# Optimization experiments

Measured on AMD Instinct MI355X. Metric: run time of the kernel, lower is better.

The kernel has to match this reference:

```python
import jax, jax.numpy as jnp
import numpy as np
import math

SCALES = [1, 2, 4, 8]
H = 1024           # hidden_size
NS = len(SCALES)
DS = H // NS       # per-scale dim = 256
NH_S = max(1, 8 // NS)  # heads per scale = 2


def _avg_pool(x, s):
    # x: [B, L, d], kernel=stride=s (L divisible by s)
    B, L, d = x.shape
    return x.reshape(B, L // s, s, d).mean(axis=2)


def _mha(q, k, v, in_w, in_b, out_w, out_b, nh):
    # torch nn.MultiheadAttention, batch_first, no mask.
    d = q.shape[-1]
    wq, wk, wv = in_w[:d], in_w[d:2 * d], in_w[2 * d:]
    bq, bk, bv = in_b[:d], in_b[d:2 * d], in_b[2 * d:]
    qh = q @ wq.T + bq
    kh = k @ wk.T + bk
    vh = v @ wv.T + bv
    B, Lq, _ = qh.shape
    Lk = kh.shape[1]
    hd = d // nh
    qh = qh.reshape(B, Lq, nh, hd).transpose(0, 2, 1, 3)
    kh = kh.reshape(B, Lk, nh, hd).transpose(0, 2, 1, 3)
    vh = vh.reshape(B, Lk, nh, hd).transpose(0, 2, 1, 3)
    scores = jnp.einsum('bhqd,bhkd->bhqk', qh, kh) * (1.0 / math.sqrt(hd))
    w = jax.nn.softmax(scores, axis=-1)
    out = jnp.einsum('bhqk,bhkd->bhqd', w, vh)
    out = out.transpose(0, 2, 1, 3).reshape(B, Lq, d)
    out = out @ out_w.T + out_b
    return out, w.mean(axis=1)  # averaged attn weights (torch default)


def setup_inputs() -> dict:
    key = jax.random.key(0)
    ks = jax.random.split(key, 20)
    B, S = 4, 2048
    f = lambda k, shape: (jax.random.normal(k, shape, dtype=jnp.float32) * 0.02)
    return {
        'query': jax.random.normal(ks[0], (B, S, H), dtype=jnp.float32),
        'key': jax.random.normal(ks[1], (B, S, H), dtype=jnp.float32),
        'value': jax.random.normal(ks[2], (B, S, H), dtype=jnp.float32),
        'wq': f(ks[3], (H, H)), 'bq': f(ks[4], (H,)),
        'wk': f(ks[5], (H, H)), 'bk': f(ks[6], (H,)),
        'wv': f(ks[7], (H, H)), 'bv': f(ks[8], (H,)),
        'mha_in_w': f(ks[9], (NS, 3 * DS, DS)),
        'mha_in_b': f(ks[10], (NS, 3 * DS)),
        'mha_out_w': f(ks[11], (NS, DS, DS)),
        'mha_out_b': f(ks[12], (NS, DS)),
        'fus_w': f(ks[13], (H, H)), 'fus_b': f(ks[14], (H,)),
    }


def reference(query, key, value, wq, bq, wk, bk, wv, bv,
              mha_in_w, mha_in_b, mha_out_w, mha_out_b, fus_w, fus_b):
    q = query @ wq.T + bq
    k = key @ wk.T + bk
    v = value @ wv.T + bv
    outs = []
    weights0 = None
    for i, s in enumerate(SCALES):
        qs = q[..., i * DS:(i + 1) * DS]
        ks_ = k[..., i * DS:(i + 1) * DS]
        vs = v[..., i * DS:(i + 1) * DS]
        if s > 1:
            ks_ = _avg_pool(ks_, s)
            vs = _avg_pool(vs, s)
        attended, w = _mha(qs, ks_, vs, mha_in_w[i], mha_in_b[i],
                           mha_out_w[i], mha_out_b[i], NH_S)
        # F.interpolate back to seq_len is an identity here (query length == seq_len)
        outs.append(attended)
        if i == 0:
            weights0 = w
    fused = jnp.concatenate(outs, axis=-1) @ fus_w.T + fus_b
    return fused, weights0
```

## Files before the change

kernel.cpp:

```cpp
#include <hip/hip_runtime.h>
#include <stdint.h>

typedef unsigned short u16;
typedef __bf16 v8bf __attribute__((ext_vector_type(8)));
typedef float v4f __attribute__((ext_vector_type(4)));
typedef __attribute__((address_space(3))) unsigned lds_t;
typedef const __attribute__((address_space(1))) unsigned g_t;

__device__ __forceinline__ u16 f2bf(float f) {
  union { float f; unsigned u; } v; v.f = f;
  unsigned r = v.u + 0x7FFFu + ((v.u >> 16) & 1u);
  return (u16)(r >> 16);
}
__device__ __forceinline__ float bf2f(u16 h) {
  union { unsigned u; float f; } v; v.u = ((unsigned)h) << 16;
  return v.f;
}
__device__ __forceinline__ ushort4 f4bf(float4 f) {
  ushort4 o;
  o.x = f2bf(f.x); o.y = f2bf(f.y); o.z = f2bf(f.z); o.w = f2bf(f.w);
  return o;
}

__global__ void k_cvt(const float* __restrict__ s, u16* __restrict__ d, long n) {
  long i = ((long)blockIdx.x * blockDim.x + threadIdx.x) * 4;
  long stride = (long)gridDim.x * blockDim.x * 4;
  for (; i < n; i += stride) {
    *(ushort4*)(d + i) = f4bf(*(const float4*)(s + i));
  }
}

__global__ void k_cvtpool(const float* __restrict__ src, u16* __restrict__ dst) {
  int g = blockIdx.x & 255, b = blockIdx.x >> 8;
  int c = threadIdx.x * 4;
  const float* p = src + ((long)b * 2048 + g * 8) * 1024 + c;
  u16* df = dst + ((long)b * 2048 + g * 8) * 1024 + c;
  float4 x[8];
#pragma unroll
  for (int j = 0; j < 8; j++) {
    x[j] = *(const float4*)(p + (long)j * 1024);
    *(ushort4*)(df + (long)j * 1024) = f4bf(x[j]);
  }
  float4 s2[4], s4[2], s8;
#pragma unroll
  for (int j = 0; j < 4; j++) {
    s2[j].x = x[2 * j].x + x[2 * j + 1].x;
    s2[j].y = x[2 * j].y + x[2 * j + 1].y;
    s2[j].z = x[2 * j].z + x[2 * j + 1].z;
    s2[j].w = x[2 * j].w + x[2 * j + 1].w;
  }
#pragma unroll
  for (int j = 0; j < 2; j++) {
    s4[j].x = s2[2 * j].x + s2[2 * j + 1].x;
    s4[j].y = s2[2 * j].y + s2[2 * j + 1].y;
    s4[j].z = s2[2 * j].z + s2[2 * j + 1].z;
    s4[j].w = s2[2 * j].w + s2[2 * j + 1].w;
  }
  s8.x = s4[0].x + s4[1].x; s8.y = s4[0].y + s4[1].y;
  s8.z = s4[0].z + s4[1].z; s8.w = s4[0].w + s4[1].w;
  u16* d2 = dst + ((long)8192 + b * 1024 + g * 4) * 1024 + c;
#pragma unroll
  for (int j = 0; j < 4; j++) {
    float4 t = {s2[j].x * 0.5f, s2[j].y * 0.5f, s2[j].z * 0.5f, s2[j].w * 0.5f};
    *(ushort4*)(d2 + (long)j * 1024) = f4bf(t);
  }
  u16* d4 = dst + ((long)12288 + b * 512 + g * 2) * 1024 + c;
#pragma unroll
  for (int j = 0; j < 2; j++) {
    float4 t = {s4[j].x * 0.25f, s4[j].y * 0.25f, s4[j].z * 0.25f, s4[j].w * 0.25f};
    *(ushort4*)(d4 + (long)j * 1024) = f4bf(t);
  }
  float4 t8 = {s8.x * 0.125f, s8.y * 0.125f, s8.z * 0.125f, s8.w * 0.125f};
  *(ushort4*)(dst + ((long)14336 + b * 256 + g) * 1024 + c) = f4bf(t8);
}

__global__ void k_tc(const float* __restrict__ src, u16* __restrict__ dst, int R, int C) {
  __shared__ float t[32][33];
  long zoff = (long)blockIdx.z * R * C;
  int r0 = blockIdx.y * 32, c0 = blockIdx.x * 32;
  int tx = threadIdx.x & 31, ty = threadIdx.x >> 5;
#pragma unroll
  for (int j = 0; j < 32; j += 8)
    t[ty + j][tx] = src[zoff + (long)(r0 + ty + j) * C + c0 + tx];
  __syncthreads();
#pragma unroll
  for (int j = 0; j < 32; j += 8)
    dst[zoff + (long)(c0 + ty + j) * R + r0 + tx] = f2bf(t[tx][ty + j]);
}

__global__ void k_bcomb_qkv(const float* __restrict__ in_w, const float* __restrict__ in_b,
                            const float* __restrict__ bq, const float* __restrict__ bk,
                            const float* __restrict__ bv, float* __restrict__ out) {
  int gw = (blockIdx.x * 256 + threadIdx.x) >> 6;
  int lane = threadIdx.x & 63;
  int p = gw >> 10, j = gw & 1023, i = j >> 8, of = j & 255;
  const float* bp = p == 0 ? bq : p == 1 ? bk : bv;
  const float* row = in_w + ((long)i * 768 + p * 256 + of) * 256;
  float s = 0.f;
#pragma unroll
  for (int m = 0; m < 4; m++) s += row[lane + m * 64] * bp[i * 256 + lane + m * 64];
#pragma unroll
  for (int m = 32; m >= 1; m >>= 1) s += __shfl_xor(s, m, 64);
  if (lane == 0) out[gw] = in_b[(long)i * 768 + p * 256 + of] + s;
}

__global__ void k_bcomb_f(const float* __restrict__ fw, const float* __restrict__ fb,
                          const float* __restrict__ ob, float* __restrict__ out) {
  int w = (blockIdx.x * 256 + threadIdx.x) >> 6;
  int lane = threadIdx.x & 63;
  const float* row = fw + (long)w * 1024;
  float s = 0.f;
  for (int k = lane; k < 1024; k += 64) s += row[k] * ob[k];
#pragma unroll
  for (int m = 32; m >= 1; m >>= 1) s += __shfl_xor(s, m, 64);
  if (lane == 0) out[w] = fb[w] + s;
}

template<int KS>
__global__ __launch_bounds__(256) void k_ksum(const float* __restrict__ P,
                                              u16* __restrict__ O, long n, int coloff) {
  long i = ((long)blockIdx.x * 256 + threadIdx.x) * 4;
  if (i >= n) return;
  float4 s = *(const float4*)(P + i);
#pragma unroll
  for (int ks = 1; ks < KS; ks++) {
    float4 t = *(const float4*)(P + (long)ks * n + i);
    s.x += t.x; s.y += t.y; s.z += t.z; s.w += t.w;
  }
  *(ushort4*)(O + (i >> 8) * 1024 + coloff + (int)(i & 255)) = f4bf(s);
}

__global__ __launch_bounds__(256) void k_ml0(
    const u16* __restrict__ QHf, const u16* __restrict__ KH,
    float* __restrict__ Mp, float* __restrict__ Lp)
{
  int kc = blockIdx.x;
  int z = blockIdx.z;
  int b = z >> 1, h = z & 1;
  int q0 = blockIdx.y * 64;
  __shared__ u16 KV[2][128][32];
  __shared__ float red[2][4][64];

  const int tid = threadIdx.x, lane = tid & 63, wave = tid >> 6;
  const int q4 = lane >> 4, l16 = lane & 15;
  const int wr = (wave >> 1) * 32, wc = (wave & 1) * 64;
  const int srow = wave * 16 + (lane >> 2), scol = (lane & 3) * 8;
  const float alpha = 0.08838834764831845f;

  v8bf qf[2][4];
#pragma unroll
  for (int mi = 0; mi < 2; mi++)
#pragma unroll
    for (int sub = 0; sub < 4; sub++)
      qf[mi][sub] = *(const v8bf*)(QHf + ((long)b * 2048 + q0 + wr + mi * 16 + l16) * 1024
                                   + h * 128 + sub * 32 + q4 * 8);

  const u16* gK = KH + (long)b * 2048 * 256 + h * 128;
  auto stageK = [&](int buf, int kt, int sub) {
    const u16* g = gK + (long)(kt * 128 + srow) * 256 + sub * 32 + scol;
    __builtin_amdgcn_global_load_lds((g_t*)g, (lds_t*)&KV[buf][wave * 16][0], 16, 0, 0);
    __builtin_amdgcn_global_load_lds((g_t*)(g + 64 * 256), (lds_t*)&KV[buf][64 + wave * 16][0], 16, 0, 0);
  };

  float m_run[2][4], l_run[2][4];
#pragma unroll
  for (int mi = 0; mi < 2; mi++)
#pragma unroll
    for (int i4 = 0; i4 < 4; i4++) { m_run[mi][i4] = -1e30f; l_run[mi][i4] = 0.f; }

  for (int kt = kc * 2; kt < kc * 2 + 2; kt++) {
    v4f s[2][4];
#pragma unroll
    for (int mi = 0; mi < 2; mi++)
#pragma unroll
      for (int ni = 0; ni < 4; ni++) s[mi][ni] = (v4f){0.f, 0.f, 0.f, 0.f};
    stageK(0, kt, 0);
    __syncthreads();
    int cur = 0;
#pragma unroll
    for (int sub = 0; sub < 4; sub++) {
      if (sub < 3) stageK(cur ^ 1, kt, sub + 1);
      v8bf kf[4];
#pragma unroll
      for (int ni = 0; ni < 4; ni++)
        kf[ni] = *(const v8bf*)&KV[cur][wc + ni * 16 + l16][q4 * 8];
#pragma unroll
      for (int mi = 0; mi < 2; mi++)
#pragma unroll
        for (int ni = 0; ni < 4; ni++)
          s[mi][ni] = __builtin_amdgcn_mfma_f32_16x16x32_bf16(qf[mi][sub], kf[ni], s[mi][ni], 0, 0, 0);
      __syncthreads();
      cur ^= 1;
    }
#pragma unroll
    for (int mi = 0; mi < 2; mi++)
#pragma unroll
      for (int ni = 0; ni < 4; ni++) s[mi][ni] *= alpha;
    float mloc[2][4];
#pragma unroll
    for (int mi = 0; mi < 2; mi++)
#pragma unroll
      for (int i4 = 0; i4 < 4; i4++)
        mloc[mi][i4] = fmaxf(fmaxf(s[mi][0][i4], s[mi][1][i4]),
                             fmaxf(s[mi][2][i4], s[mi][3][i4]));
#pragma unroll
    for (int d = 1; d <= 8; d <<= 1)
#pragma unroll
      for (int mi = 0; mi < 2; mi++)
#pragma unroll
        for (int i4 = 0; i4 < 4; i4++)
          mloc[mi][i4] = fmaxf(mloc[mi][i4], __shfl_xor(mloc[mi][i4], d, 64));
    if (l16 == 0) {
#pragma unroll
      for (int mi = 0; mi < 2; mi++)
#pragma unroll
        for (int i4 = 0; i4 < 4; i4++)
          red[0][wave][wr + mi * 16 + q4 * 4 + i4] = mloc[mi][i4];
    }
    __syncthreads();
    float lloc[2][4] = {{0.f, 0.f, 0.f, 0.f}, {0.f, 0.f, 0.f, 0.f}};
#pragma unroll
    for (int mi = 0; mi < 2; mi++)
#pragma unroll
      for (int i4 = 0; i4 < 4; i4++) {
        int rr = wr + mi * 16 + q4 * 4 + i4;
        float mn = fmaxf(fmaxf(red[0][wave][rr], red[0][wave ^ 1][rr]), m_run[mi][i4]);
        float scl = __expf(m_run[mi][i4] - mn);
        m_run[mi][i4] = mn;
        l_run[mi][i4] *= scl;
#pragma unroll
        for (int ni = 0; ni < 4; ni++)
          lloc[mi][i4] += __expf(s[mi][ni][i4] - mn);
      }
#pragma unroll
    for (int d = 1; d <= 8; d <<= 1)
#pragma unroll
      for (int mi = 0; mi < 2; mi++)
#pragma unroll
        for (int i4 = 0; i4 < 4; i4++)
          lloc[mi][i4] += __shfl_xor(lloc[mi][i4], d, 64);
    if (l16 == 0) {
#pragma unroll
      for (int mi = 0; mi < 2; mi++)
#pragma unroll
        for (int i4 = 0; i4 < 4; i4++)
          red[1][wave][wr + mi * 16 + q4 * 4 + i4] = lloc[mi][i4];
    }
    __syncthreads();
#pragma unroll
    for (int mi = 0; mi < 2; mi++)
#pragma unroll
      for (int i4 = 0; i4 < 4; i4++) {
        int rr = wr + mi * 16 + q4 * 4 + i4;
        l_run[mi][i4] += red[1][wave][rr] + red[1][wave ^ 1][rr];
      }
    __syncthreads();
  }

  if ((wave & 1) == 0 && l16 == 0) {
    long zo = ((long)kc * 8 + z) * 2048;
#pragma unroll
    for (int mi = 0; mi < 2; mi++)
#pragma unroll
      for (int i4 = 0; i4 < 4; i4++) {
        int r = q0 + wr + mi * 16 + q4 * 4 + i4;
        Mp[zo + r] = m_run[mi][i4];
        Lp[zo + r] = l_run[mi][i4];
      }
  }
}

__global__ __launch_bounds__(256) void k_mlcomb(
    const float* __restrict__ Mp, const float* __restrict__ Lp,
    float* __restrict__ M0, float* __restrict__ L0)
{
  long r = (long)blockIdx.x * 256 + threadIdx.x;
  float m = -1e30f;
#pragma unroll
  for (int kc = 0; kc < 8; kc++) m = fmaxf(m, Mp[kc * 16384 + r]);
  float l = 0.f;
#pragma unroll
  for (int kc = 0; kc < 8; kc++)
    l += Lp[kc * 16384 + r] * __expf(Mp[kc * 16384 + r] - m);
  M0[r] = m; L0[r] = l;
}

__global__ __launch_bounds__(256) void k_pv0(
    const u16* __restrict__ QHf, const u16* __restrict__ KH,
    const u16* __restrict__ VHT, const float* __restrict__ M0,
    const float* __restrict__ L0, float* __restrict__ PP, float* __restrict__ W0)
{
  int kc = blockIdx.x;
  int b = blockIdx.z;
  int q0 = blockIdx.y * 32;
  __shared__ u16 P[2][32][136];
  __shared__ u16 KV[2][2][128][32];

  const int tid = threadIdx.x, lane = tid & 63, wave = tid >> 6;
  const int q4 = lane >> 4, l16 = lane & 15;
  const int wr = (wave >> 1) * 16, wc = (wave & 1) * 64;
  const int srow = wave * 16 + (lane >> 2), scol = (lane & 3) * 8;
  const float alpha = 0.08838834764831845f;

  float mv[2][4], il[2][4];
#pragma unroll
  for (int h = 0; h < 2; h++)
#pragma unroll
    for (int i4 = 0; i4 < 4; i4++) {
      long r = (long)(b * 2 + h) * 2048 + q0 + wr + q4 * 4 + i4;
      mv[h][i4] = M0[r];
      il[h][i4] = 1.0f / L0[r];
    }

  const u16* gK = KH + (long)b * 2048 * 256;
  const u16* gQ = QHf + ((long)b * 2048 + q0 + wr + l16) * 1024;

  auto stageK2 = [&](int buf, int kt, int sub) {
#pragma unroll
    for (int h = 0; h < 2; h++) {
      const u16* g = gK + (long)(kt * 128 + srow) * 256 + h * 128 + sub * 32 + scol;
      __builtin_amdgcn_global_load_lds((g_t*)g, (lds_t*)&KV[buf][h][wave * 16][0], 16, 0, 0);
      __builtin_amdgcn_global_load_lds((g_t*)(g + 64 * 256), (lds_t*)&KV[buf][h][64 + wave * 16][0], 16, 0, 0);
    }
  };
  auto stageV2 = [&](int buf, int kt, int sub) {
#pragma unroll
    for (int h = 0; h < 2; h++) {
      const u16* g = VHT + ((long)(b * 2 + h) * 128 + srow) * 2048 + kt * 128 + sub * 32 + scol;
      __builtin_amdgcn_global_load_lds((g_t*)g, (lds_t*)&KV[buf][h][wave * 16][0], 16, 0, 0);
      __builtin_amdgcn_global_load_lds((g_t*)(g + (long)64 * 2048), (lds_t*)&KV[buf][h][64 + wave * 16][0], 16, 0, 0);
    }
  };

  v4f acc[2][4];
#pragma unroll
  for (int h = 0; h < 2; h++)
#pragma unroll
    for (int ni = 0; ni < 4; ni++) acc[h][ni] = (v4f){0.f, 0.f, 0.f, 0.f};

  for (int kt = kc * 2; kt < kc * 2 + 2; kt++) {
    v4f s[2][4];
#pragma unroll
    for (int h = 0; h < 2; h++)
#pragma unroll
      for (int ni = 0; ni < 4; ni++) s[h][ni] = (v4f){0.f, 0.f, 0.f, 0.f};
    stageK2(0, kt, 0);
    __syncthreads();
    int cur = 0;
#pragma unroll
    for (int sub = 0; sub < 4; sub++) {
      if (sub < 3) stageK2(cur ^ 1, kt, sub + 1);
      v8bf q2[2], kf[2][4];
#pragma unroll
      for (int h = 0; h < 2; h++)
        q2[h] = *(const v8bf*)(gQ + h * 128 + sub * 32 + q4 * 8);
#pragma unroll
      for (int h = 0; h < 2; h++)
#pragma unroll
        for (int ni = 0; ni < 4; ni++)
          kf[h][ni] = *(const v8bf*)&KV[cur][h][wc + ni * 16 + l16][q4 * 8];
#pragma unroll
      for (int h = 0; h < 2; h++)
#pragma unroll
        for (int ni = 0; ni < 4; ni++)
          s[h][ni] = __builtin_amdgcn_mfma_f32_16x16x32_bf16(q2[h], kf[h][ni], s[h][ni], 0, 0, 0);
      __syncthreads();
      cur ^= 1;
    }
#pragma unroll
    for (int ni = 0; ni < 4; ni++)
#pragma unroll
      for (int i4 = 0; i4 < 4; i4++) {
        float p0 = __expf(s[0][ni][i4] * alpha - mv[0][i4]) * il[0][i4];
        float p1 = __expf(s[1][ni][i4] * alpha - mv[1][i4]) * il[1][i4];
        int rr = wr + q4 * 4 + i4, cc = wc + ni * 16 + l16;
        P[0][rr][cc] = f2bf(p0);
        P[1][rr][cc] = f2bf(p1);
        W0[((long)b * 2048 + q0 + rr) * 2048 + kt * 128 + cc] = 0.5f * (p0 + p1);
      }
    stageV2(0, kt, 0);
    __syncthreads();
    int cv = 0;
#pragma unroll
    for (int sub = 0; sub < 4; sub++) {
      if (sub < 3) stageV2(cv ^ 1, kt, sub + 1);
      v8bf pf[2], vf[2][4];
#pragma unroll
      for (int h = 0; h < 2; h++)
        pf[h] = *(const v8bf*)&P[h][wr + l16][sub * 32 + q4 * 8];
#pragma unroll
      for (int h = 0; h < 2; h++)
#pragma unroll
        for (int ni = 0; ni < 4; ni++)
          vf[h][ni] = *(const v8bf*)&KV[cv][h][wc + ni * 16 + l16][q4 * 8];
#pragma unroll
      for (int h = 0; h < 2; h++)
#pragma unroll
        for (int ni = 0; ni < 4; ni++)
          acc[h][ni] = __builtin_amdgcn_mfma_f32_16x16x32_bf16(pf[h], vf[h][ni], acc[h][ni], 0, 0, 0);
      __syncthreads();
      cv ^= 1;
    }
  }

  float* pp = PP + ((long)kc * 8192 + (long)b * 2048) * 256;
#pragma unroll
  for (int h = 0; h < 2; h++)
#pragma unroll
    for (int ni = 0; ni < 4; ni++)
#pragma unroll
      for (int i4 = 0; i4 < 4; i4++) {
        int r = q0 + wr + q4 * 4 + i4;
        int c = wc + ni * 16 + l16;
        pp[(long)r * 256 + h * 128 + c] = acc[h][ni][i4];
      }
}

__global__ __launch_bounds__(256) void k_flash(
    const u16* __restrict__ QHf, const u16* __restrict__ KH,
    const u16* __restrict__ VHT, u16* __restrict__ AOf)
{
  int z = blockIdx.z;
  int i = (z >> 3) + 1;
  int b = (z >> 1) & 3, h = z & 1;
  int Ls = 2048 >> i;
  int nkt = Ls >> 7;
  long ro = (long)(16384 - (8192 >> (i - 1))) * 256;
  int q0 = blockIdx.y * 64;

  __shared__ u16 QP[64][136];
  __shared__ u16 KV[2][128][32];
  __shared__ float red[2][4][64];

  const int tid = threadIdx.x, lane = tid & 63, wave = tid >> 6;
  const int q4 = lane >> 4, l16 = lane & 15;
  const int wr = (wave >> 1) * 32, wc = (wave & 1) * 64;
  const int srow = wave * 16 + (lane >> 2);
  const int scol = (lane & 3) * 8;

  {
    const u16* gq = QHf + ((long)b * 2048 + q0) * 1024 + i * 256 + h * 128;
    int idx = tid * 4;
#pragma unroll
    for (int j = 0; j < 4; j++) {
      int r = (idx + j) >> 4, ch = (idx + j) & 15;
      *(ulonglong2*)&QP[r][ch * 8] = *(const ulonglong2*)(gq + (long)r * 1024 + ch * 8);
    }
  }
  __syncthreads();
  v8bf qf[2][4];
#pragma unroll
  for (int mi = 0; mi < 2; mi++)
#pragma unroll
    for (int sub = 0; sub < 4; sub++)
      qf[mi][sub] = *(const v8bf*)&QP[wr + mi * 16 + l16][sub * 32 + q4 * 8];
  __syncthreads();

  const u16* gK = KH + ro + (long)b * Ls * 256 + h * 128;
  const u16* gV = VHT + ro + (long)(b * 2 + h) * 128 * Ls;

  auto stageK = [&](int buf, int kt, int sub) {
    const u16* g = gK + (long)(kt * 128 + srow) * 256 + sub * 32 + scol;
    __builtin_amdgcn_global_load_lds((g_t*)g, (lds_t*)&KV[buf][wave * 16][0], 16, 0, 0);
    __builtin_amdgcn_global_load_lds((g_t*)(g + 64 * 256), (lds_t*)&KV[buf][64 + wave * 16][0], 16, 0, 0);
  };
  auto stageV = [&](int buf, int kt, int sub) {
    const u16* g = gV + (long)srow * Ls + kt * 128 + sub * 32 + scol;
    __builtin_amdgcn_global_load_lds((g_t*)g, (lds_t*)&KV[buf][wave * 16][0], 16, 0, 0);
    __builtin_amdgcn_global_load_lds((g_t*)(g + (long)64 * Ls), (lds_t*)&KV[buf][64 + wave * 16][0], 16, 0, 0);
  };

  v4f acc_o[2][4];
  float m_run[2][4], l_run[2][4];
#pragma unroll
  for (int mi = 0; mi < 2; mi++)
#pragma unroll
    for (int ni = 0; ni < 4; ni++) acc_o[mi][ni] = (v4f){0.f, 0.f, 0.f, 0.f};
#pragma unroll
  for (int mi = 0; mi < 2; mi++)
#pragma unroll
    for (int i4 = 0; i4 < 4; i4++) { m_run[mi][i4] = -1e30f; l_run[mi][i4] = 0.f; }

  const float alpha = 0.08838834764831845f;

  for (int kt = 0; kt < nkt; kt++) {
    v4f s[2][4];
#pragma unroll
    for (int mi = 0; mi < 2; mi++)
#pragma unroll
      for (int ni = 0; ni < 4; ni++) s[mi][ni] = (v4f){0.f, 0.f, 0.f, 0.f};
    stageK(0, kt, 0);
    __syncthreads();
    int cur = 0;
#pragma unroll
    for (int sub = 0; sub < 4; sub++) {
      if (sub < 3) stageK(cur ^ 1, kt, sub + 1);
      v8bf kf[4];
#pragma unroll
      for (int ni = 0; ni < 4; ni++)
        kf[ni] = *(const v8bf*)&KV[cur][wc + ni * 16 + l16][q4 * 8];
#pragma unroll
      for (int mi = 0; mi < 2; mi++)
#pragma unroll
        for (int ni = 0; ni < 4; ni++)
          s[mi][ni] = __builtin_amdgcn_mfma_f32_16x16x32_bf16(qf[mi][sub], kf[ni], s[mi][ni], 0, 0, 0);
      __syncthreads();
      cur ^= 1;
    }
    stageV(0, kt, 0);

#pragma unroll
    for (int mi = 0; mi < 2; mi++)
#pragma unroll
      for (int ni = 0; ni < 4; ni++) s[mi][ni] *= alpha;
    float mloc[2][4];
#pragma unroll
    for (int mi = 0; mi < 2; mi++)
#pragma unroll
      for (int i4 = 0; i4 < 4; i4++)
        mloc[mi][i4] = fmaxf(fmaxf(s[mi][0][i4], s[mi][1][i4]),
                             fmaxf(s[mi][2][i4], s[mi][3][i4]));
#pragma unroll
    for (int d = 1; d <= 8; d <<= 1)
#pragma unroll
      for (int mi = 0; mi < 2; mi++)
#pragma unroll
        for (int i4 = 0; i4 < 4; i4++)
          mloc[mi][i4] = fmaxf(mloc[mi][i4], __shfl_xor(mloc[mi][i4], d, 64));
    if (l16 == 0) {
#pragma unroll
      for (int mi = 0; mi < 2; mi++)
#pragma unroll
        for (int i4 = 0; i4 < 4; i4++)
          red[0][wave][wr + mi * 16 + q4 * 4 + i4] = mloc[mi][i4];
    }
    __syncthreads();
    float scl[2][4];
#pragma unroll
    for (int mi = 0; mi < 2; mi++)
#pragma unroll
      for (int i4 = 0; i4 < 4; i4++) {
        int rr = wr + mi * 16 + q4 * 4 + i4;
        float mn = fmaxf(fmaxf(red[0][wave][rr], red[0][wave ^ 1][rr]), m_run[mi][i4]);
        scl[mi][i4] = __expf(m_run[mi][i4] - mn);
        m_run[mi][i4] = mn;
      }
    float lloc[2][4] = {{0.f, 0.f, 0.f, 0.f}, {0.f, 0.f, 0.f, 0.f}};
#pragma unroll
    for (int mi = 0; mi < 2; mi++)
#pragma unroll
      for (int ni = 0; ni < 4; ni++)
#pragma unroll
        for (int i4 = 0; i4 < 4; i4++) {
          float p = __expf(s[mi][ni][i4] - m_run[mi][i4]);
          lloc[mi][i4] += p;
          QP[wr + mi * 16 + q4 * 4 + i4][wc + ni * 16 + l16] = f2bf(p);
        }
#pragma unroll
    for (int d = 1; d <= 8; d <<= 1)
#pragma unroll
      for (int mi = 0; mi < 2; mi++)
#pragma unroll
        for (int i4 = 0; i4 < 4; i4++)
          lloc[mi][i4] += __shfl_xor(lloc[mi][i4], d, 64);
    if (l16 == 0) {
#pragma unroll
      for (int mi = 0; mi < 2; mi++)
#pragma unroll
        for (int i4 = 0; i4 < 4; i4++)
          red[1][wave][wr + mi * 16 + q4 * 4 + i4] = lloc[mi][i4];
    }
#pragma unroll
    for (int mi = 0; mi < 2; mi++)
#pragma unroll
      for (int ni = 0; ni < 4; ni++)
#pragma unroll
        for (int i4 = 0; i4 < 4; i4++) acc_o[mi][ni][i4] *= scl[mi][i4];
    __syncthreads();
#pragma unroll
    for (int mi = 0; mi < 2; mi++)
#pragma unroll
      for (int i4 = 0; i4 < 4; i4++) {
        int rr = wr + mi * 16 + q4 * 4 + i4;
        l_run[mi][i4] = l_run[mi][i4] * scl[mi][i4] + red[1][wave][rr] + red[1][wave ^ 1][rr];
      }

    int cv = 0;
#pragma unroll
    for (int sub = 0; sub < 4; sub++) {
      if (sub < 3) stageV(cv ^ 1, kt, sub + 1);
      v8bf pf[2], vf[4];
#pragma unroll
      for (int mi = 0; mi < 2; mi++)
        pf[mi] = *(const v8bf*)&QP[wr + mi * 16 + l16][sub * 32 + q4 * 8];
#pragma unroll
      for (int ni = 0; ni < 4; ni++)
        vf[ni] = *(const v8bf*)&KV[cv][wc + ni * 16 + l16][q4 * 8];
#pragma unroll
      for (int mi = 0; mi < 2; mi++)
#pragma unroll
        for (int ni = 0; ni < 4; ni++)
          acc_o[mi][ni] = __builtin_amdgcn_mfma_f32_16x16x32_bf16(pf[mi], vf[ni], acc_o[mi][ni], 0, 0, 0);
      __syncthreads();
      cv ^= 1;
    }
  }

#pragma unroll
  for (int mi = 0; mi < 2; mi++)
#pragma unroll
    for (int i4 = 0; i4 < 4; i4++) {
      float inv = 1.0f / l_run[mi][i4];
#pragma unroll
      for (int ni = 0; ni < 4; ni++) {
        int r = q0 + wr + mi * 16 + q4 * 4 + i4;
        int c = wc + ni * 16 + l16;
        AOf[((long)b * 2048 + r) * 1024 + i * 256 + h * 128 + c] =
            f2bf(acc_o[mi][ni][i4] * inv);
      }
    }
}

template<int WBF>
__global__ __launch_bounds__(256) void k_gemm(
    const u16* __restrict__ A, long ldA, long sA1, long sA2,
    const u16* __restrict__ B, long ldB, long sB1, long sB2,
    void* __restrict__ Cv, long ldC, long sC1, long sC2, long sCk,
    const float* __restrict__ bias, long sBias, float alpha,
    int M, int N, int K, int nz2, int KS)
{
  __shared__ u16 As[2][128][32];
  __shared__ u16 Bs[2][128][32];
  int z = blockIdx.z;
  int ks = z % KS; int zz = z / KS;
  int z1 = zz / nz2, z2 = zz - z1 * nz2;
  A += (long)z1 * sA1 + (long)z2 * sA2 + (long)ks * K;
  B += (long)z1 * sB1 + (long)z2 * sB2 + (long)ks * K;
  long coff = (long)z1 * sC1 + (long)z2 * sC2 + (long)ks * sCk;
  const float* bz = bias ? bias + (long)z2 * sBias : nullptr;
  const int m0 = blockIdx.y * 128, n0 = blockIdx.x * 128;
  const int tid = threadIdx.x;
  const int lane = tid & 63;
  const int wave = tid >> 6;
  const int wr = (wave >> 1) * 64, wc = (wave & 1) * 64;
  const int q4 = lane >> 4, l16 = lane & 15;

  const int srow = wave * 16 + (lane >> 2);
  const int scol = (lane & 3) * 8;
  const u16* gA = A + (long)(m0 + srow) * ldA + scol;
  const u16* gB = B + (long)(n0 + srow) * ldB + scol;

  auto stage = [&](int buf, int kt) {
    __builtin_amdgcn_global_load_lds((g_t*)(gA + kt), (lds_t*)&As[buf][wave * 16][0], 16, 0, 0);
    __builtin_amdgcn_global_load_lds((g_t*)(gA + 64 * ldA + kt), (lds_t*)&As[buf][64 + wave * 16][0], 16, 0, 0);
    __builtin_amdgcn_global_load_lds((g_t*)(gB + kt), (lds_t*)&Bs[buf][wave * 16][0], 16, 0, 0);
    __builtin_amdgcn_global_load_lds((g_t*)(gB + 64 * ldB + kt), (lds_t*)&Bs[buf][64 + wave * 16][0], 16, 0, 0);
  };

  v4f acc[4][4];
#pragma unroll
  for (int i = 0; i < 4; i++)
#pragma unroll
    for (int j = 0; j < 4; j++) acc[i][j] = (v4f){0.f, 0.f, 0.f, 0.f};

  stage(0, 0);
  __syncthreads();
  int cur = 0;
  for (int kt = 0; kt < K; kt += 32) {
    if (kt + 32 < K) stage(cur ^ 1, kt + 32);
    v8bf af[4], bf[4];
#pragma unroll
    for (int i = 0; i < 4; i++) af[i] = *(const v8bf*)&As[cur][wr + i * 16 + l16][q4 * 8];
#pragma unroll
    for (int i = 0; i < 4; i++) bf[i] = *(const v8bf*)&Bs[cur][wc + i * 16 + l16][q4 * 8];
#pragma unroll
    for (int mi = 0; mi < 4; mi++)
#pragma unroll
      for (int ni = 0; ni < 4; ni++)
        acc[mi][ni] = __builtin_amdgcn_mfma_f32_16x16x32_bf16(af[mi], bf[ni], acc[mi][ni], 0, 0, 0);
    __syncthreads();
    cur ^= 1;
  }

#pragma unroll
  for (int mi = 0; mi < 4; mi++) {
    int rb = m0 + wr + mi * 16 + q4 * 4;
#pragma unroll
    for (int ni = 0; ni < 4; ni++) {
      int c = n0 + wc + ni * 16 + l16;
      float bv = bz ? bz[c] : 0.f;
#pragma unroll
      for (int i = 0; i < 4; i++) {
        int r = rb + i;
        float val = acc[mi][ni][i] * alpha + bv;
        if (WBF) ((u16*)Cv)[coff + (long)r * ldC + c] = f2bf(val);
        else     ((float*)Cv)[coff + (long)r * ldC + c] = val;
      }
    }
  }
}

__global__ __launch_bounds__(256) void k_gemm_kv(
    const u16* __restrict__ Xk, const u16* __restrict__ Xv,
    const u16* __restrict__ WCkv, const float* __restrict__ Bckv,
    u16* __restrict__ KH, u16* __restrict__ VHT)
{
  __shared__ u16 As[2][128][32];
  __shared__ u16 Bs[2][128][32];
  const int isV = blockIdx.z;
  const int m0 = blockIdx.y * 128, n0 = blockIdx.x * 128;
  const int scale = m0 < 8192 ? 0 : (m0 < 12288 ? 1 : (m0 < 14336 ? 2 : 3));
  const int rbase = scale == 0 ? 0 : (scale == 1 ? 8192 : (scale == 2 ? 12288 : 14336));
  const int lsh = 11 - scale;
  const u16* A = isV ? Xv : Xk;
  const u16* B = WCkv + (long)isV * 1048576 + (long)scale * 262144;
  const float* bz = Bckv + isV * 1024 + scale * 256;

  const int tid = threadIdx.x;
  const int lane = tid & 63, wave = tid >> 6;
  const int wr = (wave >> 1) * 64, wc = (wave & 1) * 64;
  const int q4 = lane >> 4, l16 = lane & 15;
  const int srow = wave * 16 + (lane >> 2);
  const int scol = (lane & 3) * 8;
  const u16* gA = A + (long)(m0 + srow) * 1024 + scol;
  const u16* gB = B + (long)(n0 + srow) * 1024 + scol;

  auto stage = [&](int buf, int kt) {
    __builtin_amdgcn_global_load_lds((g_t*)(gA + kt), (lds_t*)&As[buf][wave * 16][0], 16, 0, 0);
    __builtin_amdgcn_global_load_lds((g_t*)(gA + 64 * 1024 + kt), (lds_t*)&As[buf][64 + wave * 16][0], 16, 0, 0);
    __builtin_amdgcn_global_load_lds((g_t*)(gB + kt), (lds_t*)&Bs[buf][wave * 16][0], 16, 0, 0);
    __builtin_amdgcn_global_load_lds((g_t*)(gB + 64 * 1024 + kt), (lds_t*)&Bs[buf][64 + wave * 16][0], 16, 0, 0);
  };

  v4f acc[4][4];
#pragma unroll
  for (int i = 0; i < 4; i++)
#pragma unroll
    for (int j = 0; j < 4; j++) acc[i][j] = (v4f){0.f, 0.f, 0.f, 0.f};

  stage(0, 0);
  __syncthreads();
  int cur = 0;
  for (int kt = 0; kt < 1024; kt += 32) {
    if (kt + 32 < 1024) stage(cur ^ 1, kt + 32);
    v8bf af[4], bf[4];
#pragma unroll
    for (int i = 0; i < 4; i++) af[i] = *(const v8bf*)&As[cur][wr + i * 16 + l16][q4 * 8];
#pragma unroll
    for (int i = 0; i < 4; i++) bf[i] = *(const v8bf*)&Bs[cur][wc + i * 16 + l16][q4 * 8];
#pragma unroll
    for (int mi = 0; mi < 4; mi++)
#pragma unroll
      for (int ni = 0; ni < 4; ni++)
        acc[mi][ni] = __builtin_amdgcn_mfma_f32_16x16x32_bf16(af[mi], bf[ni], acc[mi][ni], 0, 0, 0);
    __syncthreads();
    cur ^= 1;
  }

#pragma unroll
  for (int mi = 0; mi < 4; mi++) {
    int rb = m0 + wr + mi * 16 + q4 * 4;
#pragma unroll
    for (int ni = 0; ni < 4; ni++) {
      int c = n0 + wc + ni * 16 + l16;
      float bv = bz[c];
#pragma unroll
      for (int i = 0; i < 4; i++) {
        int r = rb + i;
        float val = acc[mi][ni][i] + bv;
        if (!isV) {
          KH[(long)r * 256 + c] = f2bf(val);
        } else {
          int rl = r - rbase;
          int b = rl >> lsh, t = rl & ((1 << lsh) - 1);
          int h = c >> 7, n = c & 127;
          VHT[(long)rbase * 256 + (((long)(b * 2 + h) * 128 + n) << lsh) + t] = f2bf(val);
        }
      }
    }
  }
}

extern "C" void kernel_launch(void* const* d_in, const int* in_sizes, int n_in,
                              void* d_out, int out_size, void* d_ws, size_t ws_size,
                              hipStream_t stream) {
  const float* query = (const float*)d_in[0];
  const float* key_  = (const float*)d_in[1];
  const float* value = (const float*)d_in[2];
  const float* wq    = (const float*)d_in[3];
  const float* bq    = (const float*)d_in[4];
  const float* wk    = (const float*)d_in[5];
  const float* bk    = (const float*)d_in[6];
  const float* wv    = (const float*)d_in[7];
  const float* bv    = (const float*)d_in[8];
  const float* in_w  = (const float*)d_in[9];
  const float* in_b  = (const float*)d_in[10];
  const float* out_w = (const float*)d_in[11];
  const float* out_b = (const float*)d_in[12];
  const float* fus_w = (const float*)d_in[13];
  const float* fus_b = (const float*)d_in[14];
  (void)in_sizes; (void)n_in; (void)out_size; (void)ws_size;

  float* outF  = (float*)d_out;
  float* outW0 = outF + (long)4 * 2048 * 1024;

  char* base = (char*)d_ws;
  size_t off = 0;
  auto alloc = [&](size_t bytes) -> void* {
    void* p = base + off;
    off = (off + bytes + 255) & ~(size_t)255;
    return p;
  };
  const long NX = (long)8192 * 1024;
  u16* Winb = (u16*)alloc((size_t)4 * 768 * 256 * 2);
  u16* Wfb  = (u16*)alloc((size_t)1024 * 1024 * 2);
  u16* WoT  = (u16*)alloc((size_t)4 * 256 * 256 * 2);
  u16* WT   = (u16*)alloc((size_t)3 * 1024 * 1024 * 2);
  u16* WC   = (u16*)alloc((size_t)3 * 1024 * 1024 * 2);
  u16* WFc  = (u16*)alloc((size_t)1024 * 1024 * 2);
  float* Bc  = (float*)alloc((size_t)3 * 1024 * 4);
  float* fbc = (float*)alloc((size_t)1024 * 4);
  u16* Xq    = (u16*)alloc((size_t)NX * 2);
  u16* XkAll = (u16*)alloc((size_t)15360 * 1024 * 2);
  u16* XvAll = (u16*)alloc((size_t)15360 * 1024 * 2);
  u16* QHf = (u16*)alloc((size_t)8192 * 1024 * 2);
  u16* KH  = (u16*)alloc((size_t)15360 * 256 * 2);
  u16* VHT = (u16*)alloc((size_t)15360 * 256 * 2);
  float* M0 = (float*)alloc((size_t)8 * 2048 * 4);
  float* L0 = (float*)alloc((size_t)8 * 2048 * 4);
  float* Mp = (float*)alloc((size_t)8 * 8 * 2048 * 4);
  float* Lp = (float*)alloc((size_t)8 * 8 * 2048 * 4);
  float* PP = (float*)alloc((size_t)8 * 8192 * 256 * 4);
  u16* AOf = (u16*)alloc((size_t)8192 * 1024 * 2);

  const long AOsz = (long)8192 * 256;

  k_cvt<<<1024, 256, 0, stream>>>(query, Xq, NX);
  k_cvtpool<<<1024, 256, 0, stream>>>(key_,  XkAll);
  k_cvtpool<<<1024, 256, 0, stream>>>(value, XvAll);
  k_cvt<<<192, 256, 0, stream>>>(in_w, Winb, 4 * 768 * 256);
  k_cvt<<<256, 256, 0, stream>>>(fus_w, Wfb, 1024 * 1024);
  k_tc<<<dim3(32, 32, 1), 256, 0, stream>>>(wq, WT, 1024, 1024);
  k_tc<<<dim3(32, 32, 1), 256, 0, stream>>>(wk, WT + (long)1024 * 1024, 1024, 1024);
  k_tc<<<dim3(32, 32, 1), 256, 0, stream>>>(wv, WT + (long)2 * 1024 * 1024, 1024, 1024);
  k_tc<<<dim3(8, 8, 4), 256, 0, stream>>>(out_w, WoT, 256, 256);
  k_bcomb_qkv<<<768, 256, 0, stream>>>(in_w, in_b, bq, bk, bv, Bc);
  k_bcomb_f<<<256, 256, 0, stream>>>(fus_w, fus_b, out_b, fbc);

  k_gemm<1><<<dim3(8, 2, 12), 256, 0, stream>>>(
      Winb, 256, 65536, 196608,
      WT, 1024, 1048576, 256,
      WC, 1024, 1048576, 262144, 0,
      nullptr, 0, 1.f, 256, 1024, 256, 4, 1);
  k_gemm<1><<<dim3(2, 8, 4), 256, 0, stream>>>(
      Wfb, 1024, 0, 256,
      WoT, 256, 0, 65536,
      WFc, 1024, 0, 256, 0,
      nullptr, 0, 1.f, 1024, 256, 256, 4, 1);

  k_gemm<1><<<dim3(8, 64, 1), 256, 0, stream>>>(
      Xq, 1024, 0, 0, WC, 1024, 0, 0,
      QHf, 1024, 0, 0, 0, Bc, 0, 1.f, 8192, 1024, 1024, 1, 1);
  k_gemm_kv<<<dim3(2, 120, 2), 256, 0, stream>>>(
      XkAll, XvAll, WC + (long)1024 * 1024, Bc + 1024, KH, VHT);

  k_ml0<<<dim3(8, 32, 8), 256, 0, stream>>>(QHf, KH, Mp, Lp);
  k_mlcomb<<<64, 256, 0, stream>>>(Mp, Lp, M0, L0);
  k_pv0<<<dim3(8, 64, 4), 256, 0, stream>>>(QHf, KH, VHT, M0, L0, PP, outW0);
  k_ksum<8><<<2048, 256, 0, stream>>>(PP, AOf, AOsz, 0);

  k_flash<<<dim3(1, 32, 24), 256, 0, stream>>>(QHf, KH, VHT, AOf);

  k_gemm<0><<<dim3(8, 64, 1), 256, 0, stream>>>(
      AOf, 1024, 0, 0, WFc, 1024, 0, 0,
      outF, 1024, 0, 0, 0, fbc, 0, 1.f, 8192, 1024, 1024, 1, 1);
}
```

Before: 524.2 us.

## Load K/V MFMA fragments directly from global memory instead of LDS staging

Removes the double-buffered global-to-LDS staging of K and V tiles in the three attention kernels. MFMA operands are now read straight from global memory (relying on cache), which drops many __syncthreads barriers and frees LDS for higher occupancy. k_pv0 also preloads its Q fragments once into registers and double-buffers the P tile by kt parity so one barrier per tile is enough. The risk is duplicate global loads across waves and less coalesced, higher-latency operand fetches that are no longer overlapped with compute.

```diff
diff --git a/kernel.cpp b/kernel.cpp
--- a/kernel.cpp
+++ b/kernel.cpp
@@ -138,14 +138,13 @@
   int z = blockIdx.z;
   int b = z >> 1, h = z & 1;
   int q0 = blockIdx.y * 64;
-  __shared__ u16 KV[2][128][32];
   __shared__ float red[2][4][64];
 
   const int tid = threadIdx.x, lane = tid & 63, wave = tid >> 6;
   const int q4 = lane >> 4, l16 = lane & 15;
   const int wr = (wave >> 1) * 32, wc = (wave & 1) * 64;
-  const int srow = wave * 16 + (lane >> 2), scol = (lane & 3) * 8;
   const float alpha = 0.08838834764831845f;
+  (void)tid;
 
   v8bf qf[2][4];
 #pragma unroll
@@ -156,11 +155,6 @@
                                    + h * 128 + sub * 32 + q4 * 8);
 
   const u16* gK = KH + (long)b * 2048 * 256 + h * 128;
-  auto stageK = [&](int buf, int kt, int sub) {
-    const u16* g = gK + (long)(kt * 128 + srow) * 256 + sub * 32 + scol;
-    __builtin_amdgcn_global_load_lds((g_t*)g, (lds_t*)&KV[buf][wave * 16][0], 16, 0, 0);
-    __builtin_amdgcn_global_load_lds((g_t*)(g + 64 * 256), (lds_t*)&KV[buf][64 + wave * 16][0], 16, 0, 0);
-  };
 
   float m_run[2][4], l_run[2][4];
 #pragma unroll
@@ -174,23 +168,17 @@
     for (int mi = 0; mi < 2; mi++)
 #pragma unroll
       for (int ni = 0; ni < 4; ni++) s[mi][ni] = (v4f){0.f, 0.f, 0.f, 0.f};
-    stageK(0, kt, 0);
-    __syncthreads();
-    int cur = 0;
 #pragma unroll
     for (int sub = 0; sub < 4; sub++) {
-      if (sub < 3) stageK(cur ^ 1, kt, sub + 1);
       v8bf kf[4];
 #pragma unroll
       for (int ni = 0; ni < 4; ni++)
-        kf[ni] = *(const v8bf*)&KV[cur][wc + ni * 16 + l16][q4 * 8];
+        kf[ni] = *(const v8bf*)(gK + (long)(kt * 128 + wc + ni * 16 + l16) * 256 + sub * 32 + q4 * 8);
 #pragma unroll
       for (int mi = 0; mi < 2; mi++)
 #pragma unroll
         for (int ni = 0; ni < 4; ni++)
           s[mi][ni] = __builtin_amdgcn_mfma_f32_16x16x32_bf16(qf[mi][sub], kf[ni], s[mi][ni], 0, 0, 0);
-      __syncthreads();
-      cur ^= 1;
     }
 #pragma unroll
     for (int mi = 0; mi < 2; mi++)
@@ -293,14 +281,13 @@
   int kc = blockIdx.x;
   int b = blockIdx.z;
   int q0 = blockIdx.y * 32;
-  __shared__ u16 P[2][32][136];
-  __shared__ u16 KV[2][2][128][32];
+  __shared__ u16 P[2][2][32][136];
 
   const int tid = threadIdx.x, lane = tid & 63, wave = tid >> 6;
   const int q4 = lane >> 4, l16 = lane & 15;
   const int wr = (wave >> 1) * 16, wc = (wave & 1) * 64;
-  const int srow = wave * 16 + (lane >> 2), scol = (lane & 3) * 8;
   const float alpha = 0.08838834764831845f;
+  (void)tid; (void)wave;
 
   float mv[2][4], il[2][4];
 #pragma unroll
@@ -313,24 +300,13 @@
     }
 
   const u16* gK = KH + (long)b * 2048 * 256;
-  const u16* gQ = QHf + ((long)b * 2048 + q0 + wr + l16) * 1024;
-
-  auto stageK2 = [&](int buf, int kt, int sub) {
-#pragma unroll
-    for (int h = 0; h < 2; h++) {
-      const u16* g = gK + (long)(kt * 128 + srow) * 256 + h * 128 + sub * 32 + scol;
-      __builtin_amdgcn_global_load_lds((g_t*)g, (lds_t*)&KV[buf][h][wave * 16][0], 16, 0, 0);
-      __builtin_amdgcn_global_load_lds((g_t*)(g + 64 * 256), (lds_t*)&KV[buf][h][64 + wave * 16][0], 16, 0, 0);
-    }
-  };
-  auto stageV2 = [&](int buf, int kt, int sub) {
-#pragma unroll
-    for (int h = 0; h < 2; h++) {
-      const u16* g = VHT + ((long)(b * 2 + h) * 128 + srow) * 2048 + kt * 128 + sub * 32 + scol;
-      __builtin_amdgcn_global_load_lds((g_t*)g, (lds_t*)&KV[buf][h][wave * 16][0], 16, 0, 0);
-      __builtin_amdgcn_global_load_lds((g_t*)(g + (long)64 * 2048), (lds_t*)&KV[buf][h][64 + wave * 16][0], 16, 0, 0);
-    }
-  };
+  v8bf qf[2][4];
+#pragma unroll
+  for (int h = 0; h < 2; h++)
+#pragma unroll
+    for (int sub = 0; sub < 4; sub++)
+      qf[h][sub] = *(const v8bf*)(QHf + ((long)b * 2048 + q0 + wr + l16) * 1024
+                                  + h * 128 + sub * 32 + q4 * 8);
 
   v4f acc[2][4];
 #pragma unroll
@@ -339,33 +315,26 @@
     for (int ni = 0; ni < 4; ni++) acc[h][ni] = (v4f){0.f, 0.f, 0.f, 0.f};
 
   for (int kt = kc * 2; kt < kc * 2 + 2; kt++) {
+    int pb = kt & 1;
     v4f s[2][4];
 #pragma unroll
     for (int h = 0; h < 2; h++)
 #pragma unroll
       for (int ni = 0; ni < 4; ni++) s[h][ni] = (v4f){0.f, 0.f, 0.f, 0.f};
-    stageK2(0, kt, 0);
-    __syncthreads();
-    int cur = 0;
 #pragma unroll
     for (int sub = 0; sub < 4; sub++) {
-      if (sub < 3) stageK2(cur ^ 1, kt, sub + 1);
-      v8bf q2[2], kf[2][4];
+      v8bf kf[2][4];
 #pragma unroll
       for (int h = 0; h < 2; h++)
-        q2[h] = *(const v8bf*)(gQ + h * 128 + sub * 32 + q4 * 8);
+#pragma unroll
+        for (int ni = 0; ni < 4; ni++)
+          kf[h][ni] = *(const v8bf*)(gK + (long)(kt * 128 + wc + ni * 16 + l16) * 256
+                                     + h * 128 + sub * 32 + q4 * 8);
 #pragma unroll
       for (int h = 0; h < 2; h++)
 #pragma unroll
         for (int ni = 0; ni < 4; ni++)
-          kf[h][ni] = *(const v8bf*)&KV[cur][h][wc + ni * 16 + l16][q4 * 8];
-#pragma unroll
-      for (int h = 0; h < 2; h++)
-#pragma unroll
-        for (int ni = 0; ni < 4; ni++)
-          s[h][ni] = __builtin_amdgcn_mfma_f32_16x16x32_bf16(q2[h], kf[h][ni], s[h][ni], 0, 0, 0);
-      __syncthreads();
-      cur ^= 1;
+          s[h][ni] = __builtin_amdgcn_mfma_f32_16x16x32_bf16(qf[h][sub], kf[h][ni], s[h][ni], 0, 0, 0);
     }
 #pragma unroll
     for (int ni = 0; ni < 4; ni++)
@@ -374,32 +343,28 @@
         float p0 = __expf(s[0][ni][i4] * alpha - mv[0][i4]) * il[0][i4];
         float p1 = __expf(s[1][ni][i4] * alpha - mv[1][i4]) * il[1][i4];
         int rr = wr + q4 * 4 + i4, cc = wc + ni * 16 + l16;
-        P[0][rr][cc] = f2bf(p0);
-        P[1][rr][cc] = f2bf(p1);
+        P[pb][0][rr][cc] = f2bf(p0);
+        P[pb][1][rr][cc] = f2bf(p1);
         W0[((long)b * 2048 + q0 + rr) * 2048 + kt * 128 + cc] = 0.5f * (p0 + p1);
       }
-    stageV2(0, kt, 0);
     __syncthreads();
-    int cv = 0;
 #pragma unroll
     for (int sub = 0; sub < 4; sub++) {
-      if (sub < 3) stageV2(cv ^ 1, kt, sub + 1);
       v8bf pf[2], vf[2][4];
 #pragma unroll
       for (int h = 0; h < 2; h++)
-        pf[h] = *(const v8bf*)&P[h][wr + l16][sub * 32 + q4 * 8];
+        pf[h] = *(const v8bf*)&P[pb][h][wr + l16][sub * 32 + q4 * 8];
 #pragma unroll
       for (int h = 0; h < 2; h++)
 #pragma unroll
         for (int ni = 0; ni < 4; ni++)
-          vf[h][ni] = *(const v8bf*)&KV[cv][h][wc + ni * 16 + l16][q4 * 8];
+          vf[h][ni] = *(const v8bf*)(VHT + ((long)(b * 2 + h) * 128 + wc + ni * 16 + l16) * 2048
+                                     + kt * 128 + sub * 32 + q4 * 8);
 #pragma unroll
       for (int h = 0; h < 2; h++)
 #pragma unroll
         for (int ni = 0; ni < 4; ni++)
           acc[h][ni] = __builtin_amdgcn_mfma_f32_16x16x32_bf16(pf[h], vf[h][ni], acc[h][ni], 0, 0, 0);
-      __syncthreads();
-      cv ^= 1;
     }
   }
 
@@ -429,14 +394,11 @@
   int q0 = blockIdx.y * 64;
 
   __shared__ u16 QP[64][136];
-  __shared__ u16 KV[2][128][32];
   __shared__ float red[2][4][64];
 
   const int tid = threadIdx.x, lane = tid & 63, wave = tid >> 6;
   const int q4 = lane >> 4, l16 = lane & 15;
   const int wr = (wave >> 1) * 32, wc = (wave & 1) * 64;
-  const int srow = wave * 16 + (lane >> 2);
-  const int scol = (lane & 3) * 8;
 
   {
     const u16* gq = QHf + ((long)b * 2048 + q0) * 1024 + i * 256 + h * 128;
@@ -459,17 +421,6 @@
   const u16* gK = KH + ro + (long)b * Ls * 256 + h * 128;
   const u16* gV = VHT + ro + (long)(b * 2 + h) * 128 * Ls;
 
-  auto stageK = [&](int buf, int kt, int sub) {
-    const u16* g = gK + (long)(kt * 128 + srow) * 256 + sub * 32 + scol;
-    __builtin_amdgcn_global_load_lds((g_t*)g, (lds_t*)&KV[buf][wave * 16][0], 16, 0, 0);
-    __builtin_amdgcn_global_load_lds((g_t*)(g + 64 * 256), (lds_t*)&KV[buf][64 + wave * 16][0], 16, 0, 0);
-  };
-  auto stageV = [&](int buf, int kt, int sub) {
-    const u16* g = gV + (long)srow * Ls + kt * 128 + sub * 32 + scol;
-    __builtin_amdgcn_global_load_lds((g_t*)g, (lds_t*)&KV[buf][wave * 16][0], 16, 0, 0);
-    __builtin_amdgcn_global_load_lds((g_t*)(g + (long)64 * Ls), (lds_t*)&KV[buf][64 + wave * 16][0], 16, 0, 0);
-  };
-
   v4f acc_o[2][4];
   float m_run[2][4], l_run[2][4];
 #pragma unroll
@@ -489,25 +440,18 @@
     for (int mi = 0; mi < 2; mi++)
 #pragma unroll
       for (int ni = 0; ni < 4; ni++) s[mi][ni] = (v4f){0.f, 0.f, 0.f, 0.f};
-    stageK(0, kt, 0);
-    __syncthreads();
-    int cur = 0;
 #pragma unroll
     for (int sub = 0; sub < 4; sub++) {
-      if (sub < 3) stageK(cur ^ 1, kt, sub + 1);
       v8bf kf[4];
 #pragma unroll
       for (int ni = 0; ni < 4; ni++)
-        kf[ni] = *(const v8bf*)&KV[cur][wc + ni * 16 + l16][q4 * 8];
+        kf[ni] = *(const v8bf*)(gK + (long)(kt * 128 + wc + ni * 16 + l16) * 256 + sub * 32 + q4 * 8);
 #pragma unroll
       for (int mi = 0; mi < 2; mi++)
 #pragma unroll
         for (int ni = 0; ni < 4; ni++)
           s[mi][ni] = __builtin_amdgcn_mfma_f32_16x16x32_bf16(qf[mi][sub], kf[ni], s[mi][ni], 0, 0, 0);
-      __syncthreads();
-      cur ^= 1;
-    }
-    stageV(0, kt, 0);
+    }
 
 #pragma unroll
     for (int mi = 0; mi < 2; mi++)
@@ -585,24 +529,20 @@
         l_run[mi][i4] = l_run[mi][i4] * scl[mi][i4] + red[1][wave][rr] + red[1][wave ^ 1][rr];
       }
 
-    int cv = 0;
 #pragma unroll
     for (int sub = 0; sub < 4; sub++) {
-      if (sub < 3) stageV(cv ^ 1, kt, sub + 1);
       v8bf pf[2], vf[4];
 #pragma unroll
       for (int mi = 0; mi < 2; mi++)
         pf[mi] = *(const v8bf*)&QP[wr + mi * 16 + l16][sub * 32 + q4 * 8];
 #pragma unroll
       for (int ni = 0; ni < 4; ni++)
-        vf[ni] = *(const v8bf*)&KV[cv][wc + ni * 16 + l16][q4 * 8];
+        vf[ni] = *(const v8bf*)(gV + (long)(wc + ni * 16 + l16) * Ls + kt * 128 + sub * 32 + q4 * 8);
 #pragma unroll
       for (int mi = 0; mi < 2; mi++)
 #pragma unroll
         for (int ni = 0; ni < 4; ni++)
           acc_o[mi][ni] = __builtin_amdgcn_mfma_f32_16x16x32_bf16(pf[mi], vf[ni], acc_o[mi][ni], 0, 0, 0);
-      __syncthreads();
-      cv ^= 1;
     }
   }
 
```

Measured after the change: 616.9 us. 1.18x slower.
